# Kernel optimization log

Hardware: AMD Instinct MI355X
Metric: run time of the kernel (lower is better)

## Reference

```python
import jax, jax.numpy as jnp
import numpy as np

B, T, E, H = 8, 2048, 256, 8
D = E // H  # head_size = 32
EPS = 1e-5  # torch LayerNorm default


def _layernorm(x, g, b):
    m = jnp.mean(x, axis=-1, keepdims=True)
    v = jnp.var(x, axis=-1, keepdims=True)
    return (x - m) / jnp.sqrt(v + EPS) * g + b


def setup_inputs() -> dict:
    key = jax.random.key(0)
    ks = jax.random.split(key, 9)
    s = lambda k, shape, fan: (jax.random.normal(k, shape, jnp.float32) / np.sqrt(fan)).astype(jnp.float32)
    return {
        "x": jax.random.normal(ks[0], (B, T, E), jnp.float32),
        "wq": s(ks[1], (H, E, D), E),
        "wk": s(ks[2], (H, E, D), E),
        "wv": s(ks[3], (H, E, D), E),
        "w_lin": s(ks[4], (E, E), E),
        "b_lin": jnp.zeros((E,), jnp.float32),
        "g1": jnp.ones((E,), jnp.float32),
        "beta1": jnp.zeros((E,), jnp.float32),
        "g2": jnp.ones((E,), jnp.float32),
        "beta2": jnp.zeros((E,), jnp.float32),
        "w_f1": s(ks[5], (E, 4 * E), E),
        "b_f1": jnp.zeros((4 * E,), jnp.float32),
        "w_f2": s(ks[6], (4 * E, E), 4 * E),
        "b_f2": jnp.zeros((E,), jnp.float32),
    }


def reference(x, wq, wk, wv, w_lin, b_lin, g1, beta1, g2, beta2, w_f1, b_f1, w_f2, b_f2):
    b, t, e = x.shape
    xn = _layernorm(x, g1, beta1)  # norm1
    # all heads at once: (B,T,E) x (H,E,D) -> (B,H,T,D)
    q = jnp.einsum('bte,hed->bhtd', xn, wq)
    k = jnp.einsum('bte,hed->bhtd', xn, wk)
    v = jnp.einsum('bte,hed->bhtd', xn, wv)
    # scale uses C = embedding_size (as in source, not head_size)
    scores = jnp.einsum('bhtd,bhsd->bhts', q, k) * (e ** -0.5)
    mask = jnp.tril(jnp.ones((t, t), bool))  # (query t, key s)
    scores = jnp.where(mask[None, None, :, :], scores, -jnp.inf)
    # source applies softmax over dim=1 of (B,T,T) = the QUERY axis -> axis 2 of bhts
    attn = jax.nn.softmax(scores, axis=2)
    heads = jnp.einsum('bhts,bhsd->bhtd', attn, v)
    heads = heads.transpose(0, 2, 1, 3).reshape(b, t, e)  # concat over heads
    xh = xn + heads  # residual around attention
    xl = xh @ w_lin + b_lin  # projection (dropout is identity at eval)
    x2 = _layernorm(xl, g2, beta2)  # norm2
    ff = jax.nn.relu(x2 @ w_f1 + b_f1) @ w_f2 + b_f2  # FFN (dropout identity)
    return x2 + ff
```

## Files before the change

kernel.cpp:

```cpp
#include <hip/hip_runtime.h>
#include <math.h>

#define TT 2048
#define TE 256
#define NTOK 16384
#define QSCALE (0.0625f * 1.44269504088896f)

typedef short  bf16x8 __attribute__((ext_vector_type(8)));
typedef float  f32x4  __attribute__((ext_vector_type(4)));
typedef float  f32x16 __attribute__((ext_vector_type(16)));
typedef unsigned short u16x4 __attribute__((ext_vector_type(4)));
typedef unsigned short u16x8 __attribute__((ext_vector_type(8)));

__device__ __forceinline__ unsigned short f2b(float f) {
    union { float f; unsigned int u; } v; v.f = f;
    unsigned int r = v.u + 0x7FFF + ((v.u >> 16) & 1);
    return (unsigned short)(r >> 16);
}
__device__ __forceinline__ float b2f(unsigned short u) {
    union { unsigned int i; float f; } v; v.i = ((unsigned int)u) << 16;
    return v.f;
}
#if __has_builtin(__builtin_amdgcn_cvt_pk_bf16_f32)
__device__ __forceinline__ unsigned int pk_bf16(float a, float b) {
    typedef __bf16 bf2 __attribute__((ext_vector_type(2)));
    union { bf2 v; unsigned int u; } u;
    u.v = __builtin_amdgcn_cvt_pk_bf16_f32(a, b);
    return u.u;
}
#else
__device__ __forceinline__ unsigned int pk_bf16(float a, float b) {
    return (unsigned int)f2b(a) | ((unsigned int)f2b(b) << 16);
}
#endif
#if __has_builtin(__builtin_amdgcn_exp2f)
#define FEXP2(x) __builtin_amdgcn_exp2f(x)
#else
#define FEXP2(x) __expf(0.69314718056f * (x))
#endif
__device__ __forceinline__ void pswap(unsigned &a, unsigned &b) {
#if __has_builtin(__builtin_amdgcn_permlane32_swap)
    auto r = __builtin_amdgcn_permlane32_swap(a, b, false, false);
    a = r[0]; b = r[1];
#else
    asm("v_permlane32_swap_b32 %0, %1" : "+v"(a), "+v"(b));
#endif
}
__device__ __forceinline__ bf16x8 ld8(const unsigned short* p) {
    return *(const bf16x8*)p;
}
__device__ __forceinline__ void gl_lds16(const unsigned short* g, unsigned short* l) {
    __builtin_amdgcn_global_load_lds(
        (const __attribute__((address_space(1))) unsigned int*)(uintptr_t)g,
        (__attribute__((address_space(3))) unsigned int*)(uintptr_t)l,
        16, 0, 0);
}
#define MFMA16(a, b, c) __builtin_amdgcn_mfma_f32_16x16x32_bf16((a), (b), (c), 0, 0, 0)
#define MFMA32(a, b, c) __builtin_amdgcn_mfma_f32_32x32x16_bf16((a), (b), (c), 0, 0, 0)


__global__ __launch_bounds__(256) void conv_w(const float* __restrict__ wq,
                                              const float* __restrict__ wk,
                                              const float* __restrict__ wv,
                                              const float* __restrict__ w_lin,
                                              const float* __restrict__ w_f1,
                                              const float* __restrict__ w_f2,
                                              unsigned short* __restrict__ Wqkv,
                                              unsigned short* __restrict__ Wlin,
                                              unsigned short* __restrict__ Wf1,
                                              unsigned short* __restrict__ Wf2) {
    int idx = blockIdx.x * 256 + threadIdx.x;
    if (idx < 196608) {
        int n = idx >> 8, k = idx & 255;
        int which = n >> 8, h = (n >> 5) & 7, d = n & 31;
        const float* w = (which == 0) ? wq : (which == 1) ? wk : wv;
        Wqkv[idx] = f2b(w[(h * 256 + k) * 32 + d]);
    } else if (idx < 262144) {
        int i = idx - 196608; int n = i >> 8, k = i & 255;
        Wlin[i] = f2b(w_lin[k * 256 + n]);
    } else if (idx < 524288) {
        int i = idx - 262144; int n = i >> 8, k = i & 255;
        Wf1[i] = f2b(w_f1[k * 1024 + n]);
    } else {
        int i = idx - 524288; int n = i >> 10, k = i & 1023;
        Wf2[i] = f2b(w_f2[k * 256 + n]);
    }
}

__global__ __launch_bounds__(256) void ln_w(const float* __restrict__ X,
                                            const float* __restrict__ g,
                                            const float* __restrict__ bta,
                                            float* __restrict__ Y,
                                            unsigned short* __restrict__ Yb) {
    int row = blockIdx.x * 4 + (threadIdx.x >> 6);
    int lane = threadIdx.x & 63;
    const float4 v = *(const float4*)&X[(size_t)row * TE + lane * 4];
    float s = v.x + v.y + v.z + v.w;
    float s2 = v.x * v.x + v.y * v.y + v.z * v.z + v.w * v.w;
#pragma unroll
    for (int off = 1; off <= 32; off <<= 1) {
        s  += __shfl_xor(s,  off, 64);
        s2 += __shfl_xor(s2, off, 64);
    }
    float mean = s * (1.0f / TE);
    float var = s2 * (1.0f / TE) - mean * mean;
    float rstd = rsqrtf(var + 1e-5f);
    const float4 gg = *(const float4*)&g[lane * 4];
    const float4 bb = *(const float4*)&bta[lane * 4];
    float4 o;
    o.x = (v.x - mean) * rstd * gg.x + bb.x;
    o.y = (v.y - mean) * rstd * gg.y + bb.y;
    o.z = (v.z - mean) * rstd * gg.z + bb.z;
    o.w = (v.w - mean) * rstd * gg.w + bb.w;
    if (Y) *(float4*)&Y[(size_t)row * TE + lane * 4] = o;
    if (Yb) {
        u16x4 ob = { f2b(o.x), f2b(o.y), f2b(o.z), f2b(o.w) };
        *(u16x4*)&Yb[(size_t)row * TE + lane * 4] = ob;
    }
}

__global__ __launch_bounds__(256) void ln2_red(const float* __restrict__ Pp,
                                               const float* __restrict__ bias,
                                               const float* __restrict__ g,
                                               const float* __restrict__ bta,
                                               unsigned short* __restrict__ Yb) {
    const size_t SL = (size_t)NTOK * TE;
    int row = blockIdx.x * 4 + (threadIdx.x >> 6);
    int lane = threadIdx.x & 63;
    size_t base = (size_t)row * TE + lane * 4;
    const float4 p0 = *(const float4*)&Pp[base];
    const float4 p1 = *(const float4*)&Pp[SL + base];
    const float4 bl = *(const float4*)&bias[lane * 4];
    float4 v;
    v.x = p0.x + p1.x + bl.x; v.y = p0.y + p1.y + bl.y;
    v.z = p0.z + p1.z + bl.z; v.w = p0.w + p1.w + bl.w;
    float s = v.x + v.y + v.z + v.w;
    float s2 = v.x * v.x + v.y * v.y + v.z * v.z + v.w * v.w;
#pragma unroll
    for (int off = 1; off <= 32; off <<= 1) {
        s  += __shfl_xor(s,  off, 64);
        s2 += __shfl_xor(s2, off, 64);
    }
    float mean = s * (1.0f / TE);
    float var = s2 * (1.0f / TE) - mean * mean;
    float rstd = rsqrtf(var + 1e-5f);
    const float4 gg = *(const float4*)&g[lane * 4];
    const float4 bb = *(const float4*)&bta[lane * 4];
    u16x4 ob = { f2b((v.x - mean) * rstd * gg.x + bb.x),
                 f2b((v.y - mean) * rstd * gg.y + bb.y),
                 f2b((v.z - mean) * rstd * gg.z + bb.z),
                 f2b((v.w - mean) * rstd * gg.w + bb.w) };
    *(u16x4*)&Yb[base] = ob;
}

__global__ __launch_bounds__(256) void reduce2(const unsigned short* __restrict__ Pf,
                                               const float* __restrict__ bias,
                                               const unsigned short* __restrict__ x2b,
                                               float* __restrict__ out) {
    const size_t SL = (size_t)NTOK * TE;
    int row = blockIdx.x * 4 + (threadIdx.x >> 6);
    int lane = threadIdx.x & 63;
    size_t base = (size_t)row * TE + lane * 4;
    const float4 bl = *(const float4*)&bias[lane * 4];
    u16x4 r = *(const u16x4*)&x2b[base];
    float4 acc;
    acc.x = bl.x + b2f(r[0]); acc.y = bl.y + b2f(r[1]);
    acc.z = bl.z + b2f(r[2]); acc.w = bl.w + b2f(r[3]);
#pragma unroll
    for (int z = 0; z < 4; ++z) {
        u16x4 p = *(const u16x4*)&Pf[z * SL + base];
        acc.x += b2f(p[0]); acc.y += b2f(p[1]);
        acc.z += b2f(p[2]); acc.w += b2f(p[3]);
    }
    *(float4*)&out[base] = acc;
}

template<int KS>
__global__ __launch_bounds__(256) void gemm_lds(const unsigned short* __restrict__ A,
                                                int lda,
                                                const unsigned short* __restrict__ Bt,
                                                int ldb,
                                                const float* __restrict__ bias,
                                                float* __restrict__ outF,
                                                unsigned short* __restrict__ outB,
                                                int N, int relu) {
    __shared__ unsigned short Al[128 * 32];
    __shared__ unsigned short Bl[128 * 32];
    int tid = threadIdx.x;
    int w = tid >> 6, lane = tid & 63, q = lane >> 4, col = lane & 15;
    int wm = w & 1, wn = w >> 1;
    int m0 = blockIdx.x * 128;
    int n0 = blockIdx.y * 128;
    int koff = blockIdx.z * KS;
    size_t zoff = (size_t)blockIdx.z * NTOK * N;
    f32x4 acc[4][4] = {};
    int srow = lane >> 2;
    int skq  = (lane & 3) * 8;
    const unsigned short* Ag0 = A  + (size_t)(m0 + w * 32 + srow) * lda + koff + skq;
    const unsigned short* Ag1 = Ag0 + (size_t)16 * lda;
    const unsigned short* Bg0 = Bt + (size_t)(n0 + w * 32 + srow) * ldb + koff + skq;
    const unsigned short* Bg1 = Bg0 + (size_t)16 * ldb;
    unsigned short* Asl0 = &Al[(w * 32) * 32];
    unsigned short* Asl1 = Asl0 + 16 * 32;
    unsigned short* Bsl0 = &Bl[(w * 32) * 32];
    unsigned short* Bsl1 = Bsl0 + 16 * 32;
    for (int k0 = 0; k0 < KS; k0 += 32) {
        gl_lds16(Ag0 + k0, Asl0);
        gl_lds16(Ag1 + k0, Asl1);
        gl_lds16(Bg0 + k0, Bsl0);
        gl_lds16(Bg1 + k0, Bsl1);
        __syncthreads();
        bf16x8 a[4], b[4];
#pragma unroll
        for (int i = 0; i < 4; ++i)
            a[i] = ld8(&Al[(wm * 64 + i * 16 + col) * 32 + q * 8]);
#pragma unroll
        for (int j = 0; j < 4; ++j)
            b[j] = ld8(&Bl[(wn * 64 + j * 16 + col) * 32 + q * 8]);
#pragma unroll
        for (int i = 0; i < 4; ++i)
#pragma unroll
            for (int j = 0; j < 4; ++j)
                acc[i][j] = MFMA16(a[i], b[j], acc[i][j]);
        __syncthreads();
    }
#pragma unroll
    for (int i = 0; i < 4; ++i)
#pragma unroll
    for (int j = 0; j < 4; ++j) {
        int n = n0 + wn * 64 + j * 16 + col;
#pragma unroll
        for (int r = 0; r < 4; ++r) {
            int m = m0 + wm * 64 + i * 16 + q * 4 + r;
            float v = acc[i][j][r];
            if (bias) v += bias[n];
            if (relu) v = fmaxf(v, 0.f);
            if (outF) outF[zoff + (size_t)m * N + n] = v;
            if (outB) outB[zoff + (size_t)m * N + n] = f2b(v);
        }
    }
}

__global__ __launch_bounds__(256) void gemm_qkv(const unsigned short* __restrict__ A,
                                                const unsigned short* __restrict__ Bt,
                                                unsigned short* __restrict__ Qd,
                                                unsigned short* __restrict__ Kd,
                                                unsigned short* __restrict__ Vc) {
    const int K = 256;
    __shared__ unsigned short Al[128 * 32];
    __shared__ unsigned short Bl[128 * 32];
    int tid = threadIdx.x;
    int w = tid >> 6, lane = tid & 63, q = lane >> 4, col = lane & 15;
    int wm = w & 1, wn = w >> 1;
    int m0 = blockIdx.x * 128;
    int n0 = blockIdx.y * 128;
    f32x4 acc[4][4] = {};
    int srow = lane >> 2;
    int skq  = (lane & 3) * 8;
    const unsigned short* Ag0 = A  + (size_t)(m0 + w * 32 + srow) * K + skq;
    const unsigned short* Ag1 = Ag0 + (size_t)16 * K;
    const unsigned short* Bg0 = Bt + (size_t)(n0 + w * 32 + srow) * K + skq;
    const unsigned short* Bg1 = Bg0 + (size_t)16 * K;
    unsigned short* Asl0 = &Al[(w * 32) * 32];
    unsigned short* Asl1 = Asl0 + 16 * 32;
    unsigned short* Bsl0 = &Bl[(w * 32) * 32];
    unsigned short* Bsl1 = Bsl0 + 16 * 32;
    for (int k0 = 0; k0 < K; k0 += 32) {
        gl_lds16(Ag0 + k0, Asl0);
        gl_lds16(Ag1 + k0, Asl1);
        gl_lds16(Bg0 + k0, Bsl0);
        gl_lds16(Bg1 + k0, Bsl1);
        __syncthreads();
        bf16x8 a[4], b[4];
#pragma unroll
        for (int i = 0; i < 4; ++i)
            a[i] = ld8(&Al[(wm * 64 + i * 16 + col) * 32 + q * 8]);
#pragma unroll
        for (int j = 0; j < 4; ++j)
            b[j] = ld8(&Bl[(wn * 64 + j * 16 + col) * 32 + q * 8]);
#pragma unroll
        for (int i = 0; i < 4; ++i)
#pragma unroll
            for (int j = 0; j < 4; ++j)
                acc[i][j] = MFMA16(a[i], b[j], acc[i][j]);
        __syncthreads();
    }
#pragma unroll
    for (int i = 0; i < 4; ++i)
#pragma unroll
    for (int j = 0; j < 4; ++j) {
        int n = n0 + wn * 64 + j * 16 + col;
        int which = n >> 8, h = (n >> 5) & 7, d = n & 31;
        int m = m0 + wm * 64 + i * 16 + q * 4;
        int b = m >> 11, t = m & 2047;
        int bh = b * 8 + h;
        if (which == 0) {
            size_t qb = ((size_t)(bh * 2 + (d >> 4)) * TT + t) * 16 + (d & 15);
#pragma unroll
            for (int r = 0; r < 4; ++r)
                Qd[qb + r * 16] = f2b(acc[i][j][r] * QSCALE);
        } else if (which == 1) {
            size_t kb = ((size_t)(bh * 2 + (d >> 4)) * TT + t) * 16 + (d & 15);
#pragma unroll
            for (int r = 0; r < 4; ++r)
                Kd[kb + r * 16] = f2b(acc[i][j][r]);
        } else {
            uint2 pv;
            pv.x = pk_bf16(acc[i][j][0], acc[i][j][1]);
            pv.y = pk_bf16(acc[i][j][2], acc[i][j][3]);
            *(uint2*)&Vc[(((size_t)bh * 256 + (t >> 3)) * 32 + d) * 8 + (t & 7)] = pv;
        }
    }
}

__global__ __launch_bounds__(256, 4) void attn_cols(const unsigned short* __restrict__ Qd,
                                                    const unsigned short* __restrict__ Kd,
                                                    float* __restrict__ colLinv) {
    __shared__ float Lb[4][32];
    int tid = threadIdx.x;
    int w = tid >> 6, lane = tid & 63, hi = lane >> 5, l31 = lane & 31;
    int bh = blockIdx.x;
    int u = blockIdx.y;
    const unsigned short* Qb = Qd + ((size_t)bh * 2 * TT + l31) * 16 + hi * 8;
    const unsigned short* Kb = Kd + ((size_t)bh * 2 * TT + l31) * 16 + hi * 8;
    const f32x16 z16 = {};
#pragma unroll
    for (int phase = 0; phase < 2; ++phase) {
        int stile = phase ? (63 - u) : u;
        int sbase = stile * 32;
        bf16x8 a0 = ld8(Kb + (size_t)sbase * 16);
        bf16x8 a1 = ld8(Kb + ((size_t)TT + sbase) * 16);
        float acc[16] = {};
        for (int ct = stile + w; ct < 64; ct += 4) {
            int t0 = ct * 32;
            bf16x8 q0 = ld8(Qb + (size_t)t0 * 16);
            bf16x8 q1 = ld8(Qb + ((size_t)TT + t0) * 16);
            f32x16 st = MFMA32(a0, q0, z16);
            st = MFMA32(a1, q1, st);
            if (ct == stile) {
#pragma unroll
                for (int r = 0; r < 16; ++r) {
                    int s_local = (r & 3) + 8 * (r >> 2) + 4 * hi;
                    acc[r] += (l31 >= s_local) ? FEXP2(st[r]) : 0.f;
                }
            } else {
#pragma unroll
                for (int r = 0; r < 16; ++r) acc[r] += FEXP2(st[r]);
            }
        }
#pragma unroll
        for (int off = 1; off <= 16; off <<= 1)
#pragma unroll
            for (int r = 0; r < 16; ++r) acc[r] += __shfl_xor(acc[r], off, 64);
        if (l31 == 0) {
#pragma unroll
            for (int r = 0; r < 16; ++r) {
                int s_local = (r & 3) + 8 * (r >> 2) + 4 * hi;
                Lb[w][s_local] = acc[r];
            }
        }
        __syncthreads();
        if (tid < 32) {
            float s = Lb[0][tid] + Lb[1][tid] + Lb[2][tid] + Lb[3][tid];
            colLinv[(size_t)bh * TT + sbase + tid] = 1.0f / s;
        }
        __syncthreads();
    }
}

__global__ __launch_bounds__(256) void scale_vt(unsigned short* __restrict__ Vc,
                                                const float* __restrict__ colLinv) {
    int bh = blockIdx.x >> 5, g = blockIdx.x & 31;
    int sb = g * 8 + (threadIdx.x >> 5);
    int d = threadIdx.x & 31;
    size_t base = (((size_t)bh * 256 + sb) * 32 + d) * 8;
    u16x8 v = *(const u16x8*)&Vc[base];
    const float4 i0 = *(const float4*)&colLinv[(size_t)bh * TT + sb * 8];
    const float4 i1 = *(const float4*)&colLinv[(size_t)bh * TT + sb * 8 + 4];
    u16x8 o;
    o[0] = f2b(b2f(v[0]) * i0.x); o[1] = f2b(b2f(v[1]) * i0.y);
    o[2] = f2b(b2f(v[2]) * i0.z); o[3] = f2b(b2f(v[3]) * i0.w);
    o[4] = f2b(b2f(v[4]) * i1.x); o[5] = f2b(b2f(v[5]) * i1.y);
    o[6] = f2b(b2f(v[6]) * i1.z); o[7] = f2b(b2f(v[7]) * i1.w);
    *(u16x8*)&Vc[base] = o;
}

__global__ __launch_bounds__(256, 4) void attn_out(const unsigned short* __restrict__ Qd,
                                                   const unsigned short* __restrict__ Kd,
                                                   const unsigned short* __restrict__ Vc,
                                                   const unsigned short* __restrict__ xnb,
                                                   unsigned short* __restrict__ xh_bf) {
    __shared__ float Ob[4][32][36];
    int tid = threadIdx.x;
    int w = tid >> 6, lane = tid & 63, hi = lane >> 5, l31 = lane & 31;
    int bh = blockIdx.x, b = bh >> 3, h = bh & 7;
    int u = blockIdx.y;
    const unsigned short* Kb = Kd + ((size_t)bh * 2 * TT + l31) * 16 + hi * 8;
    const unsigned short* Vb = Vc + (size_t)bh * 65536 + hi * 256 + l31 * 8;
    const unsigned short* Qbase = Qd + ((size_t)bh * 2 * TT + l31) * 16 + hi * 8;
    const f32x16 z16 = {};

#pragma unroll
    for (int phase = 0; phase < 2; ++phase) {
        int tt = phase ? (63 - u) : u;
        int tbase = tt * 32;
        bf16x8 q0 = ld8(Qbase + (size_t)tbase * 16);
        bf16x8 q1 = ld8(Qbase + ((size_t)TT + tbase) * 16);
        f32x16 acc = z16;

        int c = w;
        bf16x8 ka0 = ld8(Kb + (size_t)c * 512);
        bf16x8 ka1 = ld8(Kb + (size_t)TT * 16 + (size_t)c * 512);
        bf16x8 vv0 = ld8(Vb + (size_t)c * 1024);
        bf16x8 vv1 = ld8(Vb + (size_t)c * 1024 + 512);

        for (; c <= tt; c += 4) {
            bool diag = (c == tt);
            f32x16 st = MFMA32(ka0, q0, z16);
            st = MFMA32(ka1, q1, st);
            int cn = c + 4;
            if (cn <= tt) {
                ka0 = ld8(Kb + (size_t)cn * 512);
                ka1 = ld8(Kb + (size_t)TT * 16 + (size_t)cn * 512);
            }
            unsigned Wd[8];
            if (diag) {
#pragma unroll
                for (int j = 0; j < 8; ++j) {
                    int r0 = 2 * j;
                    int s0 = (r0 & 3) + 8 * (r0 >> 2) + 4 * hi;
                    float e0 = (s0 <= l31)     ? FEXP2(st[r0])     : 0.f;
                    float e1 = (s0 + 1 <= l31) ? FEXP2(st[r0 + 1]) : 0.f;
                    Wd[j] = pk_bf16(e0, e1);
                }
            } else {
#pragma unroll
                for (int j = 0; j < 8; ++j)
                    Wd[j] = pk_bf16(FEXP2(st[2 * j]), FEXP2(st[2 * j + 1]));
            }
            pswap(Wd[0], Wd[2]); pswap(Wd[1], Wd[3]);
            pswap(Wd[4], Wd[6]); pswap(Wd[5], Wd[7]);
            union { unsigned u4[4]; bf16x8 v; } pa0, pa1;
            pa0.u4[0] = Wd[0]; pa0.u4[1] = Wd[1]; pa0.u4[2] = Wd[2]; pa0.u4[3] = Wd[3];
            pa1.u4[0] = Wd[4]; pa1.u4[1] = Wd[5]; pa1.u4[2] = Wd[6]; pa1.u4[3] = Wd[7];
            acc = MFMA32(pa0.v, vv0, acc);
            acc = MFMA32(pa1.v, vv1, acc);
            if (cn <= tt) {
                vv0 = ld8(Vb + (size_t)cn * 1024);
                vv1 = ld8(Vb + (size_t)cn * 1024 + 512);
            }
        }

#pragma unroll
        for (int r = 0; r < 16; ++r) {
            int t = (r & 3) + 8 * (r >> 2) + 4 * hi;
            Ob[w][t][l31] = acc[r];
        }
        __syncthreads();
        {
            int row = tid >> 3;
            int c4 = (tid & 7) * 4;
            float4 s0 = *(const float4*)&Ob[0][row][c4];
            float4 s1 = *(const float4*)&Ob[1][row][c4];
            float4 s2 = *(const float4*)&Ob[2][row][c4];
            float4 s3 = *(const float4*)&Ob[3][row][c4];
            size_t base = ((size_t)(b * TT) + tbase + row) * TE + h * 32 + c4;
            u16x4 xv = *(const u16x4*)&xnb[base];
            u16x4 ob = { f2b(s0.x + s1.x + s2.x + s3.x + b2f(xv[0])),
                         f2b(s0.y + s1.y + s2.y + s3.y + b2f(xv[1])),
                         f2b(s0.z + s1.z + s2.z + s3.z + b2f(xv[2])),
                         f2b(s0.w + s1.w + s2.w + s3.w + b2f(xv[3])) };
            *(u16x4*)&xh_bf[base] = ob;
        }
        __syncthreads();
    }
}

extern "C" void kernel_launch(void* const* d_in, const int* in_sizes, int n_in,
                              void* d_out, int out_size, void* d_ws, size_t ws_size,
                              hipStream_t stream) {
    (void)in_sizes; (void)n_in; (void)out_size; (void)ws_size;
    const float* x     = (const float*)d_in[0];
    const float* wq    = (const float*)d_in[1];
    const float* wk    = (const float*)d_in[2];
    const float* wv    = (const float*)d_in[3];
    const float* w_lin = (const float*)d_in[4];
    const float* b_lin = (const float*)d_in[5];
    const float* g1    = (const float*)d_in[6];
    const float* beta1 = (const float*)d_in[7];
    const float* g2    = (const float*)d_in[8];
    const float* beta2 = (const float*)d_in[9];
    const float* w_f1  = (const float*)d_in[10];
    const float* b_f1  = (const float*)d_in[11];
    const float* w_f2  = (const float*)d_in[12];
    const float* b_f2  = (const float*)d_in[13];
    float* out = (float*)d_out;

    char* ws = (char*)d_ws;
    unsigned short* Wqkv_t = (unsigned short*)(ws + 0);
    unsigned short* Wlin_t = (unsigned short*)(ws + 393216);
    unsigned short* Wf1_t  = (unsigned short*)(ws + 524288);
    unsigned short* Wf2_t  = (unsigned short*)(ws + 1048576);
    float*          colLinv= (float*)(ws + 1572864);
    unsigned short* xn_bf  = (unsigned short*)(ws + 2097152);
    unsigned short* Qbf    = (unsigned short*)(ws + 10485760);
    unsigned short* Kbf    = (unsigned short*)(ws + 18874368);
    unsigned short* Vt     = (unsigned short*)(ws + 27262976);
    unsigned short* xh_bf  = (unsigned short*)(ws + 35651584);
    float*          Pp     = (float*)(ws + 44040192);
    unsigned short* Pf     = (unsigned short*)(ws + 44040192);
    unsigned short* x2_bf  = xn_bf;
    unsigned short* h_bf   = Qbf;

    conv_w<<<3072, 256, 0, stream>>>(wq, wk, wv, w_lin, w_f1, w_f2,
                                     Wqkv_t, Wlin_t, Wf1_t, Wf2_t);
    ln_w<<<4096, 256, 0, stream>>>(x, g1, beta1, nullptr, xn_bf);
    gemm_qkv<<<dim3(128, 6), 256, 0, stream>>>(xn_bf, Wqkv_t, Qbf, Kbf, Vt);
    attn_cols<<<dim3(64, 32), 256, 0, stream>>>(Qbf, Kbf, colLinv);
    scale_vt<<<2048, 256, 0, stream>>>(Vt, colLinv);
    attn_out<<<dim3(64, 32), 256, 0, stream>>>(Qbf, Kbf, Vt, xn_bf, xh_bf);
    gemm_lds<128><<<dim3(128, 2, 2), 256, 0, stream>>>(xh_bf, 256, Wlin_t, 256,
                                                       nullptr, Pp, nullptr, 256, 0);
    ln2_red<<<4096, 256, 0, stream>>>(Pp, b_lin, g2, beta2, x2_bf);
    gemm_lds<256><<<dim3(128, 8, 1), 256, 0, stream>>>(x2_bf, 256, Wf1_t, 256,
                                                       b_f1, nullptr, h_bf, 1024, 1);
    gemm_lds<256><<<dim3(128, 2, 4), 256, 0, stream>>>(h_bf, 1024, Wf2_t, 1024,
                                                       nullptr, nullptr, Pf, 256, 0);
    reduce2<<<4096, 256, 0, stream>>>(Pf, b_f2, x2_bf, out);
}
```

Baseline: 262.9 us.

## Double-buffer LDS tiles and XOR-swizzle layout in GEMM kernels

Both LDS-staged GEMM kernels (generic and QKV projection) now keep two shared-memory buffers, so the global-to-LDS load for the next K slice is issued while MFMAs run on the current one. This drops one barrier per iteration. The LDS layout is XOR-swizzled on both the write side (global source column chosen per row) and the read side, to cut bank conflicts on the 16-byte fragment loads. The cost is twice the LDS per block, which may lower occupancy. Correctness relies on the two swizzle functions matching.

After: 262.8 us. Within noise of the previous version (-0.1%).

```diff
diff --git a/kernel.cpp b/kernel.cpp
--- a/kernel.cpp
+++ b/kernel.cpp
@@ -184,8 +184,8 @@
                                                 float* __restrict__ outF,
                                                 unsigned short* __restrict__ outB,
                                                 int N, int relu) {
-    __shared__ unsigned short Al[128 * 32];
-    __shared__ unsigned short Bl[128 * 32];
+    __shared__ unsigned short Al[2][128 * 32];
+    __shared__ unsigned short Bl[2][128 * 32];
     int tid = threadIdx.x;
     int w = tid >> 6, lane = tid & 63, q = lane >> 4, col = lane & 15;
     int wm = w & 1, wn = w >> 1;
@@ -195,35 +195,40 @@
     size_t zoff = (size_t)blockIdx.z * NTOK * N;
     f32x4 acc[4][4] = {};
     int srow = lane >> 2;
-    int skq  = (lane & 3) * 8;
+    int skq  = ((lane & 3) ^ ((srow >> 1) & 3)) * 8;
     const unsigned short* Ag0 = A  + (size_t)(m0 + w * 32 + srow) * lda + koff + skq;
     const unsigned short* Ag1 = Ag0 + (size_t)16 * lda;
     const unsigned short* Bg0 = Bt + (size_t)(n0 + w * 32 + srow) * ldb + koff + skq;
     const unsigned short* Bg1 = Bg0 + (size_t)16 * ldb;
-    unsigned short* Asl0 = &Al[(w * 32) * 32];
-    unsigned short* Asl1 = Asl0 + 16 * 32;
-    unsigned short* Bsl0 = &Bl[(w * 32) * 32];
-    unsigned short* Bsl1 = Bsl0 + 16 * 32;
+    int rq = (q ^ ((col >> 1) & 3)) * 8;
+#define G_STAGE(cur, k0) do { \
+        gl_lds16(Ag0 + (k0), &Al[cur][(w * 32) * 32]); \
+        gl_lds16(Ag1 + (k0), &Al[cur][(w * 32 + 16) * 32]); \
+        gl_lds16(Bg0 + (k0), &Bl[cur][(w * 32) * 32]); \
+        gl_lds16(Bg1 + (k0), &Bl[cur][(w * 32 + 16) * 32]); \
+    } while (0)
+    G_STAGE(0, 0);
+    __syncthreads();
+    int cur = 0;
+#pragma unroll
     for (int k0 = 0; k0 < KS; k0 += 32) {
-        gl_lds16(Ag0 + k0, Asl0);
-        gl_lds16(Ag1 + k0, Asl1);
-        gl_lds16(Bg0 + k0, Bsl0);
-        gl_lds16(Bg1 + k0, Bsl1);
-        __syncthreads();
+        int kn = k0 + 32;
+        if (kn < KS) G_STAGE(cur ^ 1, kn);
         bf16x8 a[4], b[4];
 #pragma unroll
         for (int i = 0; i < 4; ++i)
-            a[i] = ld8(&Al[(wm * 64 + i * 16 + col) * 32 + q * 8]);
+            a[i] = ld8(&Al[cur][(wm * 64 + i * 16 + col) * 32 + rq]);
 #pragma unroll
         for (int j = 0; j < 4; ++j)
-            b[j] = ld8(&Bl[(wn * 64 + j * 16 + col) * 32 + q * 8]);
+            b[j] = ld8(&Bl[cur][(wn * 64 + j * 16 + col) * 32 + rq]);
 #pragma unroll
         for (int i = 0; i < 4; ++i)
 #pragma unroll
             for (int j = 0; j < 4; ++j)
                 acc[i][j] = MFMA16(a[i], b[j], acc[i][j]);
-        __syncthreads();
-    }
+        if (kn < KS) { __syncthreads(); cur ^= 1; }
+    }
+#undef G_STAGE
 #pragma unroll
     for (int i = 0; i < 4; ++i)
 #pragma unroll
@@ -247,8 +252,8 @@
                                                 unsigned short* __restrict__ Kd,
                                                 unsigned short* __restrict__ Vc) {
     const int K = 256;
-    __shared__ unsigned short Al[128 * 32];
-    __shared__ unsigned short Bl[128 * 32];
+    __shared__ unsigned short Al[2][128 * 32];
+    __shared__ unsigned short Bl[2][128 * 32];
     int tid = threadIdx.x;
     int w = tid >> 6, lane = tid & 63, q = lane >> 4, col = lane & 15;
     int wm = w & 1, wn = w >> 1;
@@ -256,35 +261,40 @@
     int n0 = blockIdx.y * 128;
     f32x4 acc[4][4] = {};
     int srow = lane >> 2;
-    int skq  = (lane & 3) * 8;
+    int skq  = ((lane & 3) ^ ((srow >> 1) & 3)) * 8;
     const unsigned short* Ag0 = A  + (size_t)(m0 + w * 32 + srow) * K + skq;
     const unsigned short* Ag1 = Ag0 + (size_t)16 * K;
     const unsigned short* Bg0 = Bt + (size_t)(n0 + w * 32 + srow) * K + skq;
     const unsigned short* Bg1 = Bg0 + (size_t)16 * K;
-    unsigned short* Asl0 = &Al[(w * 32) * 32];
-    unsigned short* Asl1 = Asl0 + 16 * 32;
-    unsigned short* Bsl0 = &Bl[(w * 32) * 32];
-    unsigned short* Bsl1 = Bsl0 + 16 * 32;
+    int rq = (q ^ ((col >> 1) & 3)) * 8;
+#define G_STAGE(cur, k0) do { \
+        gl_lds16(Ag0 + (k0), &Al[cur][(w * 32) * 32]); \
+        gl_lds16(Ag1 + (k0), &Al[cur][(w * 32 + 16) * 32]); \
+        gl_lds16(Bg0 + (k0), &Bl[cur][(w * 32) * 32]); \
+        gl_lds16(Bg1 + (k0), &Bl[cur][(w * 32 + 16) * 32]); \
+    } while (0)
+    G_STAGE(0, 0);
+    __syncthreads();
+    int cur = 0;
+#pragma unroll
     for (int k0 = 0; k0 < K; k0 += 32) {
-        gl_lds16(Ag0 + k0, Asl0);
-        gl_lds16(Ag1 + k0, Asl1);
-        gl_lds16(Bg0 + k0, Bsl0);
-        gl_lds16(Bg1 + k0, Bsl1);
-        __syncthreads();
+        int kn = k0 + 32;
+        if (kn < K) G_STAGE(cur ^ 1, kn);
         bf16x8 a[4], b[4];
 #pragma unroll
         for (int i = 0; i < 4; ++i)
-            a[i] = ld8(&Al[(wm * 64 + i * 16 + col) * 32 + q * 8]);
+            a[i] = ld8(&Al[cur][(wm * 64 + i * 16 + col) * 32 + rq]);
 #pragma unroll
         for (int j = 0; j < 4; ++j)
-            b[j] = ld8(&Bl[(wn * 64 + j * 16 + col) * 32 + q * 8]);
+            b[j] = ld8(&Bl[cur][(wn * 64 + j * 16 + col) * 32 + rq]);
 #pragma unroll
         for (int i = 0; i < 4; ++i)
 #pragma unroll
             for (int j = 0; j < 4; ++j)
                 acc[i][j] = MFMA16(a[i], b[j], acc[i][j]);
-        __syncthreads();
-    }
+        if (kn < K) { __syncthreads(); cur ^= 1; }
+    }
+#undef G_STAGE
 #pragma unroll
     for (int i = 0; i < 4; ++i)
 #pragma unroll
```
